# Performance work log

Measured on AMD Instinct MI355X. Metric: run time of the kernel, lower is better.

## Reference

```python
import jax, jax.numpy as jnp
import numpy as np

L = 2          # num_layers
D = 2048       # embed_dim
HQ = 16        # num_q_heads
HK = 4         # num_kv_heads
HD = D // HQ   # head_size = 128
G = HQ // HK   # q_to_kv_ratio = 4
P = 8192       # embed_dim_proj
V = 32000      # vocab_size
B = 1
S = 2048
EPS = 1e-5
THETA = 500000.0
NEG = -1e30


def setup_inputs() -> dict:
    key = jax.random.key(0)
    ks = jax.random.split(key, 8)
    s = 0.02
    return {
        "tokens": jax.random.randint(ks[0], (B, S), 0, V, dtype=jnp.int32),
        "embed": jax.random.normal(ks[1], (V, D), jnp.float32) * s,
        "attn_norm_w": jnp.ones((L, D), jnp.float32),
        "qkv_w": jax.random.normal(ks[2], (L, D, D + 2 * HK * HD), jnp.float32) * s,
        "attn_out_w": jax.random.normal(ks[3], (L, D, D), jnp.float32) * s,
        "mlp_norm_w": jnp.ones((L, D), jnp.float32),
        "mlp_in_w": jax.random.normal(ks[4], (L, D, 2 * P), jnp.float32) * s,
        "mlp_out_w": jax.random.normal(ks[5], (L, P, D), jnp.float32) * s,
        "final_norm_w": jnp.ones((D,), jnp.float32),
        "lm_head_w": jax.random.normal(ks[6], (D, V), jnp.float32) * s,
    }


def _rms(x, w):
    return w * (x * jax.lax.rsqrt(jnp.mean(x * x, axis=-1, keepdims=True) + EPS))


def _rope_cos_sin():
    inv = 1.0 / (THETA ** (jnp.arange(0, HD, 2, dtype=jnp.float32) / HD))  # [HD/2]
    ang = jnp.arange(S, dtype=jnp.float32)[:, None] * inv[None, :]         # [S, HD/2]
    return jnp.cos(ang), jnp.sin(ang)


def _rope(t, cos, sin):
    # t: [B,S,H,HD]; interleaved complex rotation on (even, odd) pairs
    x = t.reshape(t.shape[:-1] + (HD // 2, 2))
    x0, x1 = x[..., 0], x[..., 1]
    c = cos[None, :, None, :]
    sn = sin[None, :, None, :]
    out = jnp.stack([x0 * c - x1 * sn, x0 * sn + x1 * c], axis=-1)
    return out.reshape(t.shape)


def _layer(x, nw1, wqkv, wo, nw2, wi, wmo, cos, sin, mask):
    # attention block (pre-norm, residual)
    h = _rms(x, nw1)
    qkv = h @ wqkv
    q = qkv[..., :D].reshape(B, S, HQ, HD)
    k = qkv[..., D:D + HK * HD].reshape(B, S, HK, HD)
    v = qkv[..., D + HK * HD:].reshape(B, S, HK, HD)
    q = _rope(q, cos, sin)
    k = _rope(k, cos, sin)
    # GQA: repeat_interleave along head dim
    k = jnp.repeat(k, G, axis=2)
    v = jnp.repeat(v, G, axis=2)
    scores = jnp.einsum('bqhd,bkhd->bhqk', q, k) / np.float32(np.sqrt(HD))
    scores = jnp.where(mask, scores, NEG)
    attn = jax.nn.softmax(scores, axis=-1)
    o = jnp.einsum('bhqk,bkhd->bqhd', attn, v).reshape(B, S, D)
    x = x + o @ wo
    # SwiGLU block (pre-norm, residual)
    h = _rms(x, nw2)
    gu = h @ wi
    gate, up = gu[..., :P], gu[..., P:]
    x = x + (jax.nn.silu(gate) * up) @ wmo
    return x


def reference(tokens, embed, attn_norm_w, qkv_w, attn_out_w, mlp_norm_w,
              mlp_in_w, mlp_out_w, final_norm_w, lm_head_w):
    cos, sin = _rope_cos_sin()
    mask = jnp.tril(jnp.ones((S, S), dtype=bool))  # offset=0 prefill -> causal
    x = embed[tokens]  # [B,S,D]
    for i in range(L):
        x = _layer(x, attn_norm_w[i], qkv_w[i], attn_out_w[i],
                   mlp_norm_w[i], mlp_in_w[i], mlp_out_w[i], cos, sin, mask)
    return _rms(x, final_norm_w) @ lm_head_w  # [B,S,V]
```

## Files before the change

kernel.cpp:

```cpp
#include <hip/hip_runtime.h>
#include <math.h>

#define S_LEN 2048
#define DMODEL 2048
#define NHQ 16
#define NHK 4
#define HDIM 128
#define PDIM 8192
#define VOCAB 32000
#define NQKV 3072
#define EPSI 1e-5f

typedef unsigned short u16;
typedef unsigned int u32;
typedef __bf16 bf16x8 __attribute__((ext_vector_type(8)));
typedef float f32x4 __attribute__((ext_vector_type(4)));

__device__ __forceinline__ u16 f2bf(float f){
  u32 u = __builtin_bit_cast(u32, f);
  u += 0x7fffu + ((u >> 16) & 1u);
  return (u16)(u >> 16);
}
__device__ __forceinline__ float bf2f(u16 h){
  u32 u = ((u32)h) << 16;
  return __builtin_bit_cast(float, u);
}
__device__ __forceinline__ bf16x8 ld8(const u16* p){
  return __builtin_bit_cast(bf16x8, *(const uint4*)p);
}
__device__ __forceinline__ f32x4 mfma16(bf16x8 a, bf16x8 b, f32x4 c){
  return __builtin_amdgcn_mfma_f32_16x16x32_bf16(a, b, c, 0, 0, 0);
}

#define GLOAD_LDS16(gp, lp) __builtin_amdgcn_global_load_lds( \
    (__attribute__((address_space(1))) void*)(gp), \
    (__attribute__((address_space(3))) void*)(lp), 16, 0, 0)

__device__ __forceinline__ bf16x8 lds_frag(const u16* Lb, int R, int g){
  const int Rp = R >> 1;
  const int s8 = (((R & 1) << 2) | g) ^ (Rp & 7);
  return ld8(Lb + Rp * 64 + s8 * 8);
}
__device__ __forceinline__ void stage_sw(const u16* base, long row0, int kstride, int kt,
                                         int q, u16* Ldst_waveuniform){
  const int Rp = q >> 3;
  const int u = (q & 7) ^ (Rp & 7);
  const int R = (Rp << 1) | (u >> 2);
  const u16* gp = base + (row0 + R) * (long)kstride + kt + ((u & 3) << 3);
  GLOAD_LDS16(gp, Ldst_waveuniform);
}

__device__ __forceinline__ void map_bmn(int id0, int nwg, int nbn, int G,
                                        int& bm, int& bn){
  const int cpx = nwg >> 3;
  const int id = (id0 & 7) * cpx + (id0 >> 3);
  const int bmi = id % G;
  const int r2 = id / G;
  bn = r2 % nbn;
  bm = (r2 / nbn) * G + bmi;
}

__global__ void k_embed(const int* __restrict__ tok, const float* __restrict__ emb,
                        float* __restrict__ x){
  const int s = blockIdx.x, t = threadIdx.x;
  const long r = tok[s];
  const float4* src = (const float4*)(emb + r * DMODEL);
  float4* dst = (float4*)(x + (long)s * DMODEL);
  dst[t] = src[t];
  dst[t + 256] = src[t + 256];
}

__global__ void k_rmsnorm(const float* __restrict__ x, const float* __restrict__ w,
                          u16* __restrict__ out){
  const int s = blockIdx.x, t = threadIdx.x;
  const float4* xr = (const float4*)(x + (long)s * DMODEL);
  const float4 a = xr[t], b = xr[t + 256];
  float ss = a.x*a.x + a.y*a.y + a.z*a.z + a.w*a.w
           + b.x*b.x + b.y*b.y + b.z*b.z + b.w*b.w;
  #pragma unroll
  for (int off = 32; off > 0; off >>= 1) ss += __shfl_down(ss, off, 64);
  __shared__ float part[4];
  if ((t & 63) == 0) part[t >> 6] = ss;
  __syncthreads();
  const float r = rsqrtf((part[0] + part[1] + part[2] + part[3]) * (1.f / 2048.f) + EPSI);
  const float4* wr = (const float4*)w;
  const float4 wa = wr[t], wb = wr[t + 256];
  uint2 ua, ub;
  ua.x = (u32)f2bf(a.x*r*wa.x) | ((u32)f2bf(a.y*r*wa.y) << 16);
  ua.y = (u32)f2bf(a.z*r*wa.z) | ((u32)f2bf(a.w*r*wa.w) << 16);
  ub.x = (u32)f2bf(b.x*r*wb.x) | ((u32)f2bf(b.y*r*wb.y) << 16);
  ub.y = (u32)f2bf(b.z*r*wb.z) | ((u32)f2bf(b.w*r*wb.w) << 16);
  *(uint2*)(out + (long)s * DMODEL + 4 * t) = ua;
  *(uint2*)(out + (long)s * DMODEL + 1024 + 4 * t) = ub;
}

__global__ __launch_bounds__(256) void k_convT(const float* __restrict__ W,
                                               u16* __restrict__ Wt, int N, int K){
  const int n0 = blockIdx.x * 64, k0 = blockIdx.y * 64;
  const int t = threadIdx.x;
  __shared__ u16 T[64][72];
  const int r = t >> 4, c = (t & 15) << 2;
  #pragma unroll
  for (int p = 0; p < 4; ++p){
    const int k = p * 16 + r;
    const float4 v = *(const float4*)(W + (long)(k0 + k) * N + n0 + c);
    T[c + 0][k] = f2bf(v.x);
    T[c + 1][k] = f2bf(v.y);
    T[c + 2][k] = f2bf(v.z);
    T[c + 3][k] = f2bf(v.w);
  }
  __syncthreads();
  const int nr = t >> 3, kc = (t & 7) << 3;
  #pragma unroll
  for (int p = 0; p < 2; ++p){
    const int n = p * 32 + nr;
    *(uint4*)(Wt + (long)(n0 + n) * K + k0 + kc) = *(const uint4*)(&T[n][kc]);
  }
}

__global__ __launch_bounds__(256) void k_convTmi(const float* __restrict__ W,
                                                 u16* __restrict__ Wt, int N, int K){
  const int n0 = blockIdx.x * 64, k0 = blockIdx.y * 64;
  const int t = threadIdx.x;
  __shared__ u16 T[64][72];
  const int r = t >> 4, c = (t & 15) << 2;
  #pragma unroll
  for (int p = 0; p < 4; ++p){
    const int k = p * 16 + r;
    const float4 v = *(const float4*)(W + (long)(k0 + k) * N + n0 + c);
    T[c + 0][k] = f2bf(v.x);
    T[c + 1][k] = f2bf(v.y);
    T[c + 2][k] = f2bf(v.z);
    T[c + 3][k] = f2bf(v.w);
  }
  __syncthreads();
  int drow0;
  if (n0 < PDIM) drow0 = (n0 >> 7) * 256 + (n0 & 127);
  else { const int m0 = n0 - PDIM; drow0 = (m0 >> 7) * 256 + 128 + (m0 & 127); }
  const int nr = t >> 3, kc = (t & 7) << 3;
  #pragma unroll
  for (int p = 0; p < 2; ++p){
    const int n = p * 32 + nr;
    *(uint4*)(Wt + (long)(drow0 + n) * K + k0 + kc) = *(const uint4*)(&T[n][kc]);
  }
}

__global__ __launch_bounds__(256) void k_transV(const u16* __restrict__ qkv,
                                                u16* __restrict__ vT){
  const int s0 = blockIdx.x * 64, d0 = blockIdx.y * 64, kh = blockIdx.z;
  const int t = threadIdx.x;
  __shared__ u16 T[64][72];
  #pragma unroll
  for (int p = 0; p < 4; ++p){
    const int s = p * 16 + (t >> 4);
    const int c = (t & 15) * 4;
    const uint2 v = *(const uint2*)(qkv + (long)(s0 + s) * NQKV + DMODEL + 512 + kh * HDIM + d0 + c);
    T[c + 0][s] = (u16)(v.x);
    T[c + 1][s] = (u16)(v.x >> 16);
    T[c + 2][s] = (u16)(v.y);
    T[c + 3][s] = (u16)(v.y >> 16);
  }
  __syncthreads();
  #pragma unroll
  for (int p = 0; p < 2; ++p){
    const int d = p * 32 + (t >> 3);
    *(uint4*)(vT + ((long)kh * HDIM + d0 + d) * S_LEN + s0 + (t & 7) * 8) =
        *(const uint4*)(&T[d][(t & 7) * 8]);
  }
}

template<int OUT_BF16, int RES>
__global__ __launch_bounds__(256) void k_gemm(const u16* __restrict__ A, const u16* __restrict__ Bt,
                                              void* C, const float* Rs,
                                              int M, int N, int K, int nbn, int G){
  int bm, bn;
  map_bmn(blockIdx.x, gridDim.x, nbn, G, bm, bn);
  const int t = threadIdx.x;
  const int w = t >> 6, lane = t & 63, l15 = lane & 15, g = lane >> 4;
  const int wr = w >> 1, wc = w & 1;
  __shared__ u16 As[4096];
  __shared__ u16 Bs[4096];
  f32x4 acc[4][4] = {};
  const long arow = (long)bm * 128;
  const long brow = (long)bn * 128;
  for (int kt = 0; kt < K; kt += 32){
    __syncthreads();
    #pragma unroll
    for (int c = 0; c < 2; ++c){
      const int q0 = ((w << 1) | c) << 6;
      const int q  = q0 | lane;
      stage_sw(A,  arow, K, kt, q, As + q0 * 8);
      stage_sw(Bt, brow, K, kt, q, Bs + q0 * 8);
    }
    __syncthreads();
    bf16x8 af[4], bfr[4];
    #pragma unroll
    for (int i = 0; i < 4; ++i)
      af[i] = lds_frag(As, wr * 64 + i * 16 + l15, g);
    #pragma unroll
    for (int i = 0; i < 4; ++i)
      bfr[i] = lds_frag(Bs, wc * 64 + i * 16 + l15, g);
    #pragma unroll
    for (int mi = 0; mi < 4; ++mi)
      #pragma unroll
      for (int ni = 0; ni < 4; ++ni)
        acc[mi][ni] = mfma16(af[mi], bfr[ni], acc[mi][ni]);
  }
  const int row0 = bm * 128 + wr * 64, col0 = bn * 128 + wc * 64;
  #pragma unroll
  for (int mi = 0; mi < 4; ++mi){
    #pragma unroll
    for (int ni = 0; ni < 4; ++ni){
      #pragma unroll
      for (int r = 0; r < 4; ++r){
        const long ri = row0 + mi * 16 + g * 4 + r;
        const long ci = col0 + ni * 16 + l15;
        float v = acc[mi][ni][r];
        if (RES) v += Rs[ri * N + ci];
        if (OUT_BF16) ((u16*)C)[ri * N + ci] = f2bf(v);
        else          ((float*)C)[ri * N + ci] = v;
      }
    }
  }
}

__global__ __launch_bounds__(256) void k_gemmsk(const u16* __restrict__ A,
                                                const u16* __restrict__ Bt,
                                                float* __restrict__ P,
                                                int M, int N, int K, int nbn, int G){
  const int ks = blockIdx.y;
  const int KH = K >> 1;
  A  += (long)ks * KH;
  Bt += (long)ks * KH;
  P  += (long)ks * M * N;
  int bm, bn;
  map_bmn(blockIdx.x, gridDim.x, nbn, G, bm, bn);
  const int t = threadIdx.x;
  const int w = t >> 6, lane = t & 63, l15 = lane & 15, g = lane >> 4;
  const int wr = w >> 1, wc = w & 1;
  __shared__ u16 As[4096];
  __shared__ u16 Bs[4096];
  f32x4 acc[4][4] = {};
  const long arow = (long)bm * 128;
  const long brow = (long)bn * 128;
  for (int kt = 0; kt < KH; kt += 32){
    __syncthreads();
    #pragma unroll
    for (int c = 0; c < 2; ++c){
      const int q0 = ((w << 1) | c) << 6;
      const int q  = q0 | lane;
      stage_sw(A,  arow, K, kt, q, As + q0 * 8);
      stage_sw(Bt, brow, K, kt, q, Bs + q0 * 8);
    }
    __syncthreads();
    bf16x8 af[4], bfr[4];
    #pragma unroll
    for (int i = 0; i < 4; ++i)
      af[i] = lds_frag(As, wr * 64 + i * 16 + l15, g);
    #pragma unroll
    for (int i = 0; i < 4; ++i)
      bfr[i] = lds_frag(Bs, wc * 64 + i * 16 + l15, g);
    #pragma unroll
    for (int mi = 0; mi < 4; ++mi)
      #pragma unroll
      for (int ni = 0; ni < 4; ++ni)
        acc[mi][ni] = mfma16(af[mi], bfr[ni], acc[mi][ni]);
  }
  const int row0 = bm * 128 + wr * 64, col0 = bn * 128 + wc * 64;
  #pragma unroll
  for (int mi = 0; mi < 4; ++mi){
    #pragma unroll
    for (int ni = 0; ni < 4; ++ni){
      #pragma unroll
      for (int r = 0; r < 4; ++r){
        const long ri = row0 + mi * 16 + g * 4 + r;
        const long ci = col0 + ni * 16 + l15;
        P[ri * N + ci] = acc[mi][ni][r];
      }
    }
  }
}

__global__ void k_red2(float* __restrict__ x, const float* __restrict__ p0,
                       const float* __restrict__ p1){
  const long i = ((long)blockIdx.x * 256 + threadIdx.x) * 4;
  const float4 a = *(const float4*)(p0 + i);
  const float4 b = *(const float4*)(p1 + i);
  float4 c = *(const float4*)(x + i);
  c.x += a.x + b.x; c.y += a.y + b.y; c.z += a.z + b.z; c.w += a.w + b.w;
  *(float4*)(x + i) = c;
}

template<int OUT_BF16>
__global__ __launch_bounds__(1024, 4) void k_gemmX(const u16* __restrict__ A,
                                                   const u16* __restrict__ Bt,
                                                   void* C, int M, int N, int K){
  __shared__ u16 L[65536];
  const int t = threadIdx.x;
  const int w = t >> 6, lane = t & 63, l15 = lane & 15, g = lane >> 4;
  const int wr = w >> 2, wc = w & 3;
  const int nbm = M >> 8;
  int id = blockIdx.x;
  {
    const int cpx = gridDim.x >> 3;
    id = (id & 7) * cpx + (id >> 3);
  }
  const int bm = id % nbm, bn = id / nbm;
  const int NT = K >> 5;

  const int Rp0 = t >> 3;
  const int u0  = (t & 7) ^ (Rp0 & 7);
  const int R0  = (Rp0 << 1) | (u0 >> 2);
  const int kc0 = (u0 & 3) << 3;
  const u16* pA = A  + ((long)bm * 256 + R0) * (long)K + kc0;
  const u16* pB = Bt + ((long)bn * 256 + R0) * (long)K + kc0;
  const int w0 = (t & ~63) * 8;

  auto stage = [&](int s){
    u16* d = L + s * 16384;
    GLOAD_LDS16(pA, d + w0);
    GLOAD_LDS16(pB, d + 8192 + w0);
    pA += 32; pB += 32;
  };

  stage(0); stage(1); stage(2);
  asm volatile("s_waitcnt vmcnt(4)" ::: "memory");
  __builtin_amdgcn_s_barrier();

  f32x4 acc[4][4] = {};
  for (int tt = 0; tt < NT; ++tt){
    const int slot = tt & 3;
    const u16* sA = L + slot * 16384;
    const u16* sB = sA + 8192;
    bf16x8 af[4], bfr[4];
    #pragma unroll
    for (int mi = 0; mi < 4; ++mi)
      af[mi] = lds_frag(sA, wr * 64 + mi * 16 + l15, g);
    #pragma unroll
    for (int ni = 0; ni < 4; ++ni)
      bfr[ni] = lds_frag(sB, wc * 64 + ni * 16 + l15, g);
    if (tt + 3 < NT) stage((tt + 3) & 3);
    asm volatile("s_waitcnt lgkmcnt(0)" ::: "memory");
    if (tt + 3 < NT)      asm volatile("s_waitcnt vmcnt(4)" ::: "memory");
    else if (tt + 2 < NT) asm volatile("s_waitcnt vmcnt(2)" ::: "memory");
    else if (tt + 1 < NT) asm volatile("s_waitcnt vmcnt(0)" ::: "memory");
    __builtin_amdgcn_s_barrier();
    __builtin_amdgcn_s_setprio(1);
    #pragma unroll
    for (int mi = 0; mi < 4; ++mi)
      #pragma unroll
      for (int ni = 0; ni < 4; ++ni)
        acc[mi][ni] = mfma16(af[mi], bfr[ni], acc[mi][ni]);
    __builtin_amdgcn_s_setprio(0);
  }
  const int row0 = bm * 256 + wr * 64, col0 = bn * 256 + wc * 64;
  #pragma unroll
  for (int mi = 0; mi < 4; ++mi){
    #pragma unroll
    for (int ni = 0; ni < 4; ++ni){
      #pragma unroll
      for (int r = 0; r < 4; ++r){
        const long ri = row0 + mi * 16 + g * 4 + r;
        const long ci = col0 + ni * 16 + l15;
        const float v = acc[mi][ni][r];
        if (OUT_BF16) ((u16*)C)[ri * N + ci] = f2bf(v);
        else          ((float*)C)[ri * N + ci] = v;
      }
    }
  }
}

__global__ __launch_bounds__(1024, 4) void k_gemmXswi(const u16* __restrict__ A,
                                                      const u16* __restrict__ Bt,
                                                      u16* __restrict__ O,
                                                      int M, int K){
  __shared__ u16 L[65536];
  const int t = threadIdx.x;
  const int w = t >> 6, lane = t & 63, l15 = lane & 15, g = lane >> 4;
  const int wr = w >> 2, wc = w & 3;
  const int nbm = M >> 8;
  int id = blockIdx.x;
  {
    const int cpx = gridDim.x >> 3;
    id = (id & 7) * cpx + (id >> 3);
  }
  const int bm = id % nbm, bn = id / nbm;
  const int NT = K >> 5;

  const int Rp0 = t >> 3;
  const int u0  = (t & 7) ^ (Rp0 & 7);
  const int R0  = (Rp0 << 1) | (u0 >> 2);
  const int kc0 = (u0 & 3) << 3;
  const u16* pA = A  + ((long)bm * 256 + R0) * (long)K + kc0;
  const u16* pB = Bt + ((long)bn * 256 + R0) * (long)K + kc0;
  const int w0 = (t & ~63) * 8;

  auto stage = [&](int s){
    u16* d = L + s * 16384;
    GLOAD_LDS16(pA, d + w0);
    GLOAD_LDS16(pB, d + 8192 + w0);
    pA += 32; pB += 32;
  };

  stage(0); stage(1); stage(2);
  asm volatile("s_waitcnt vmcnt(4)" ::: "memory");
  __builtin_amdgcn_s_barrier();

  f32x4 acc[4][4] = {};
  for (int tt = 0; tt < NT; ++tt){
    const int slot = tt & 3;
    const u16* sA = L + slot * 16384;
    const u16* sB = sA + 8192;
    bf16x8 af[4], bfr[4];
    #pragma unroll
    for (int mi = 0; mi < 4; ++mi)
      af[mi] = lds_frag(sA, wr * 64 + mi * 16 + l15, g);
    #pragma unroll
    for (int ni = 0; ni < 4; ++ni)
      bfr[ni] = lds_frag(sB, wc * 64 + ni * 16 + l15, g);
    if (tt + 3 < NT) stage((tt + 3) & 3);
    asm volatile("s_waitcnt lgkmcnt(0)" ::: "memory");
    if (tt + 3 < NT)      asm volatile("s_waitcnt vmcnt(4)" ::: "memory");
    else if (tt + 2 < NT) asm volatile("s_waitcnt vmcnt(2)" ::: "memory");
    else if (tt + 1 < NT) asm volatile("s_waitcnt vmcnt(0)" ::: "memory");
    __builtin_amdgcn_s_barrier();
    __builtin_amdgcn_s_setprio(1);
    #pragma unroll
    for (int mi = 0; mi < 4; ++mi)
      #pragma unroll
      for (int ni = 0; ni < 4; ++ni)
        acc[mi][ni] = mfma16(af[mi], bfr[ni], acc[mi][ni]);
    __builtin_amdgcn_s_setprio(0);
  }
  __syncthreads();
  float* U = (float*)L;
  if (wc >= 2){
    const int base = ((wr << 1) | (wc - 2)) * 4096;
    #pragma unroll
    for (int mi = 0; mi < 4; ++mi)
      #pragma unroll
      for (int ni = 0; ni < 4; ++ni)
        #pragma unroll
        for (int r = 0; r < 4; ++r)
          U[base + (mi * 16 + g * 4 + r) * 64 + ni * 16 + l15] = acc[mi][ni][r];
  }
  __syncthreads();
  if (wc < 2){
    const int base = ((wr << 1) | wc) * 4096;
    #pragma unroll
    for (int mi = 0; mi < 4; ++mi){
      #pragma unroll
      for (int ni = 0; ni < 4; ++ni){
        #pragma unroll
        for (int r = 0; r < 4; ++r){
          const float gv = acc[mi][ni][r];
          const float uv = U[base + (mi * 16 + g * 4 + r) * 64 + ni * 16 + l15];
          const float ov = gv / (1.f + __expf(-gv)) * uv;
          const long ri = bm * 256 + wr * 64 + mi * 16 + g * 4 + r;
          const int ci = bn * 128 + wc * 64 + ni * 16 + l15;
          O[ri * PDIM + ci] = f2bf(ov);
        }
      }
    }
  }
}

__global__ void k_rope(u16* __restrict__ qkv){
  const int idx = blockIdx.x * 256 + threadIdx.x;
  const int i = idx & 63;
  const int head = (idx >> 6) % 20;
  const int s = idx / (64 * 20);
  const long base = (long)s * NQKV + (head < NHQ ? head * HDIM : DMODEL + (head - NHQ) * HDIM);
  u32* p = (u32*)(qkv + base + 2 * i);
  const u32 v = *p;
  const float x0 = bf2f((u16)(v & 0xffffu)), x1 = bf2f((u16)(v >> 16));
  const float ang = (float)s * exp2f(-0.29580575889569023f * (float)i);
  float sn, cs;
  sincosf(ang, &sn, &cs);
  const float y0 = x0 * cs - x1 * sn;
  const float y1 = x0 * sn + x1 * cs;
  *p = (u32)f2bf(y0) | ((u32)f2bf(y1) << 16);
}

__global__ __launch_bounds__(512) void k_attn(const u16* __restrict__ qkv,
                                              const u16* __restrict__ vT,
                                              u16* __restrict__ o){
  const int qb = blockIdx.x;
  const int kh = blockIdx.y >> 1;
  const int h  = (kh << 2) + ((blockIdx.y & 1) << 1) + (threadIdx.x >> 8);
  const int t = threadIdx.x, lane = t & 63, l15 = lane & 15, g = lane >> 4;
  const int ws = (t >> 6) & 3;
  const int wv = t >> 6;
  __shared__ u16 Ks[2][8192];
  __shared__ u16 Vs[2][8192];
  __shared__ u16 Ps[8][16 * 72];
  const int q0 = qb * 64 + ws * 16;
  bf16x8 aq[4];
  #pragma unroll
  for (int d0 = 0; d0 < 4; ++d0)
    aq[d0] = ld8(qkv + (long)(q0 + l15) * NQKV + h * HDIM + d0 * 32 + g * 8);
  f32x4 acc_o[8] = {};
  float mst[4], lst[4];
  #pragma unroll
  for (int r = 0; r < 4; ++r){ mst[r] = -1e30f; lst[r] = 0.f; }
  const float scale = 0.08838834764831843f;

  auto stageK = [&](int kt, int b){
    #pragma unroll
    for (int p = 0; p < 2; ++p){
      const int q = p * 512 + t;
      const int r = q >> 4, u = q & 15;
      const u16* gp = qkv + (long)(kt * 64 + r) * NQKV + DMODEL + kh * HDIM + ((u ^ (r & 15)) << 3);
      GLOAD_LDS16(gp, Ks[b] + (p * 512 + (t & ~63)) * 8);
    }
  };
  auto stageV = [&](int kt, int b){
    #pragma unroll
    for (int p = 0; p < 2; ++p){
      const int q = p * 512 + t;
      const int r = q >> 3, u = q & 7;
      const u16* gp = vT + ((long)kh * HDIM + r) * S_LEN + kt * 64 + ((u ^ (r & 7)) << 3);
      GLOAD_LDS16(gp, Vs[b] + (p * 512 + (t & ~63)) * 8);
    }
  };

  const int nkt = qb + 1;
  stageK(0, 0); stageV(0, 0);
  for (int kt = 0; kt < nkt; ++kt){
    const int kv0 = kt << 6;
    __builtin_amdgcn_s_barrier();
    if (kt + 1 < nkt){
      stageK(kt + 1, (kt + 1) & 1);
      stageV(kt + 1, (kt + 1) & 1);
      asm volatile("s_waitcnt vmcnt(4)" ::: "memory");
    } else {
      asm volatile("s_waitcnt vmcnt(0)" ::: "memory");
    }
    __builtin_amdgcn_s_barrier();
    const u16* K_ = Ks[kt & 1];
    const u16* V_ = Vs[kt & 1];
    f32x4 sacc[4] = {};
    #pragma unroll
    for (int d0 = 0; d0 < 4; ++d0){
      #pragma unroll
      for (int j2 = 0; j2 < 4; ++j2){
        const bf16x8 bk = ld8(K_ + (j2 * 16 + l15) * 128 + ((((d0 << 2) | g) ^ l15) << 3));
        sacc[j2] = mfma16(aq[d0], bk, sacc[j2]);
      }
    }
    float p[4][4], scl[4];
    #pragma unroll
    for (int r = 0; r < 4; ++r){
      const int qrow = q0 + g * 4 + r;
      float mx = -1e30f;
      #pragma unroll
      for (int j2 = 0; j2 < 4; ++j2){
        float sv = sacc[j2][r] * scale;
        sv = (kv0 + j2 * 16 + l15 <= qrow) ? sv : -1e30f;
        p[j2][r] = sv;
        mx = fmaxf(mx, sv);
      }
      #pragma unroll
      for (int off = 1; off < 16; off <<= 1) mx = fmaxf(mx, __shfl_xor(mx, off, 64));
      const float mnew = fmaxf(mst[r], mx);
      scl[r] = __expf(mst[r] - mnew);
      float rs = 0.f;
      #pragma unroll
      for (int j2 = 0; j2 < 4; ++j2){ p[j2][r] = __expf(p[j2][r] - mnew); rs += p[j2][r]; }
      #pragma unroll
      for (int off = 1; off < 16; off <<= 1) rs += __shfl_xor(rs, off, 64);
      lst[r] = lst[r] * scl[r] + rs;
      mst[r] = mnew;
    }
    #pragma unroll
    for (int n = 0; n < 8; ++n)
      #pragma unroll
      for (int r = 0; r < 4; ++r)
        acc_o[n][r] *= scl[r];
    #pragma unroll
    for (int j2 = 0; j2 < 4; ++j2)
      #pragma unroll
      for (int r = 0; r < 4; ++r)
        Ps[wv][(g * 4 + r) * 72 + j2 * 16 + l15] = f2bf(p[j2][r]);
    #pragma unroll
    for (int kk = 0; kk < 2; ++kk){
      const bf16x8 pa = ld8(Ps[wv] + l15 * 72 + kk * 32 + g * 8);
      #pragma unroll
      for (int n = 0; n < 8; ++n){
        const int row = n * 16 + l15;
        const bf16x8 bv = ld8(V_ + row * 64 + ((((kk << 2) | g) ^ (l15 & 7)) << 3));
        acc_o[n] = mfma16(pa, bv, acc_o[n]);
      }
    }
    asm volatile("s_waitcnt lgkmcnt(0)" ::: "memory");
  }
  #pragma unroll
  for (int n = 0; n < 8; ++n){
    #pragma unroll
    for (int r = 0; r < 4; ++r){
      const float ov = acc_o[n][r] / lst[r];
      o[(long)(q0 + g * 4 + r) * DMODEL + h * HDIM + n * 16 + l15] = f2bf(ov);
    }
  }
}

extern "C" void kernel_launch(void* const* d_in, const int* in_sizes, int n_in,
                              void* d_out, int out_size, void* d_ws, size_t ws_size,
                              hipStream_t stream){
  const int*   tokens       = (const int*)d_in[0];
  const float* embed        = (const float*)d_in[1];
  const float* attn_norm_w  = (const float*)d_in[2];
  const float* qkv_w        = (const float*)d_in[3];
  const float* attn_out_w   = (const float*)d_in[4];
  const float* mlp_norm_w   = (const float*)d_in[5];
  const float* mlp_in_w     = (const float*)d_in[6];
  const float* mlp_out_w    = (const float*)d_in[7];
  const float* final_norm_w = (const float*)d_in[8];
  const float* lm_head_w    = (const float*)d_in[9];

  char* ws = (char*)d_ws;
  float* xf  = (float*)(ws);
  u16* hbf   = (u16*)(ws + 16777216);
  u16* qkvb  = (u16*)(ws + 25165824);
  u16* obf   = (u16*)(ws + 37748736);
  u16* gub   = (u16*)(ws + 46137344);
  u16* hb2   = (u16*)(ws + 113246208);
  u16* wbuf  = (u16*)(ws + 146800640);
  u16* vTb   = (u16*)(ws + 277872640);
  float* pp  = (float*)gub;

  k_embed<<<S_LEN, 256, 0, stream>>>(tokens, embed, xf);
  for (int l = 0; l < 2; ++l){
    k_rmsnorm<<<S_LEN, 256, 0, stream>>>(xf, attn_norm_w + (long)l * DMODEL, hbf);
    k_convT<<<dim3(NQKV/64, DMODEL/64), 256, 0, stream>>>(
        qkv_w + (long)l * DMODEL * NQKV, wbuf, NQKV, DMODEL);
    k_gemm<1,0><<<(S_LEN/128) * (NQKV/128), 256, 0, stream>>>(
        hbf, wbuf, qkvb, nullptr, S_LEN, NQKV, DMODEL, NQKV/128, 4);
    k_rope<<<(S_LEN * 20 * 64) / 256, 256, 0, stream>>>(qkvb);
    k_transV<<<dim3(S_LEN/64, 2, 4), 256, 0, stream>>>(qkvb, vTb);
    k_attn<<<dim3(S_LEN/64, 8), 512, 0, stream>>>(qkvb, vTb, obf);
    k_convT<<<dim3(DMODEL/64, DMODEL/64), 256, 0, stream>>>(
        attn_out_w + (long)l * DMODEL * DMODEL, wbuf, DMODEL, DMODEL);
    k_gemm<0,1><<<(S_LEN/128) * (DMODEL/128), 256, 0, stream>>>(
        obf, wbuf, xf, xf, S_LEN, DMODEL, DMODEL, DMODEL/128, 4);
    k_rmsnorm<<<S_LEN, 256, 0, stream>>>(xf, mlp_norm_w + (long)l * DMODEL, hbf);
    k_convTmi<<<dim3((2*PDIM)/64, DMODEL/64), 256, 0, stream>>>(
        mlp_in_w + (long)l * DMODEL * 2 * PDIM, wbuf, 2*PDIM, DMODEL);
    k_gemmXswi<<<(S_LEN/256) * ((2*PDIM)/256), 1024, 0, stream>>>(
        hbf, wbuf, hb2, S_LEN, DMODEL);
    k_convT<<<dim3(DMODEL/64, PDIM/64), 256, 0, stream>>>(
        mlp_out_w + (long)l * PDIM * DMODEL, wbuf, DMODEL, PDIM);
    k_gemmsk<<<dim3((S_LEN/128) * (DMODEL/128), 2), 256, 0, stream>>>(
        hb2, wbuf, pp, S_LEN, DMODEL, PDIM, DMODEL/128, 2);
    k_red2<<<(S_LEN * DMODEL) / 1024, 256, 0, stream>>>(
        xf, pp, pp + (long)S_LEN * DMODEL);
  }
  k_rmsnorm<<<S_LEN, 256, 0, stream>>>(xf, final_norm_w, hbf);
  k_convT<<<dim3(VOCAB/64, DMODEL/64), 256, 0, stream>>>(lm_head_w, wbuf, VOCAB, DMODEL);
  k_gemmX<0><<<(S_LEN/256) * (VOCAB/256), 1024, 0, stream>>>(
      hbf, wbuf, (float*)d_out, S_LEN, VOCAB, DMODEL);
}
```

Measured before the change: 1.388 ms.

## Fuse split-K reduction with RMSNorm and reshape attention grid

Merges the split-K partial-sum reduction after the MLP-out GEMM with the following RMSNorm, whether that is the next layer's attention norm or the final norm. This removes a kernel launch and a re-read of the residual stream. Separately, attention blocks shrink to 256 threads, each handling one head. The grid becomes 1D: block IDs are interleaved so each XCD stays on one KV head, and query blocks are issued longest-first to balance causal work. Each block now stages K/V tiles alone, so K/V traffic per head pair doubles, but occupancy and scheduling granularity should improve.

```diff
diff --git a/kernel.cpp b/kernel.cpp
--- a/kernel.cpp
+++ b/kernel.cpp
@@ -92,6 +92,40 @@
   ub.y = (u32)f2bf(b.z*r*wb.z) | ((u32)f2bf(b.w*r*wb.w) << 16);
   *(uint2*)(out + (long)s * DMODEL + 4 * t) = ua;
   *(uint2*)(out + (long)s * DMODEL + 1024 + 4 * t) = ub;
+}
+
+__global__ void k_red2rms(float* __restrict__ x, const float* __restrict__ p0,
+                          const float* __restrict__ p1, const float* __restrict__ w,
+                          u16* __restrict__ out){
+  const int s = blockIdx.x, t = threadIdx.x;
+  const long base = (long)s * DMODEL;
+  float4 a = ((const float4*)(x + base))[t];
+  float4 b = ((const float4*)(x + base))[t + 256];
+  const float4 a0 = ((const float4*)(p0 + base))[t];
+  const float4 b0 = ((const float4*)(p0 + base))[t + 256];
+  const float4 a1 = ((const float4*)(p1 + base))[t];
+  const float4 b1 = ((const float4*)(p1 + base))[t + 256];
+  a.x += a0.x + a1.x; a.y += a0.y + a1.y; a.z += a0.z + a1.z; a.w += a0.w + a1.w;
+  b.x += b0.x + b1.x; b.y += b0.y + b1.y; b.z += b0.z + b1.z; b.w += b0.w + b1.w;
+  ((float4*)(x + base))[t] = a;
+  ((float4*)(x + base))[t + 256] = b;
+  float ss = a.x*a.x + a.y*a.y + a.z*a.z + a.w*a.w
+           + b.x*b.x + b.y*b.y + b.z*b.z + b.w*b.w;
+  #pragma unroll
+  for (int off = 32; off > 0; off >>= 1) ss += __shfl_down(ss, off, 64);
+  __shared__ float part[4];
+  if ((t & 63) == 0) part[t >> 6] = ss;
+  __syncthreads();
+  const float r = rsqrtf((part[0] + part[1] + part[2] + part[3]) * (1.f / 2048.f) + EPSI);
+  const float4* wr = (const float4*)w;
+  const float4 wa = wr[t], wb = wr[t + 256];
+  uint2 ua, ub;
+  ua.x = (u32)f2bf(a.x*r*wa.x) | ((u32)f2bf(a.y*r*wa.y) << 16);
+  ua.y = (u32)f2bf(a.z*r*wa.z) | ((u32)f2bf(a.w*r*wa.w) << 16);
+  ub.x = (u32)f2bf(b.x*r*wb.x) | ((u32)f2bf(b.y*r*wb.y) << 16);
+  ub.y = (u32)f2bf(b.z*r*wb.z) | ((u32)f2bf(b.w*r*wb.w) << 16);
+  *(uint2*)(out + base + 4 * t) = ua;
+  *(uint2*)(out + base + 1024 + 4 * t) = ub;
 }
 
 __global__ __launch_bounds__(256) void k_convT(const float* __restrict__ W,
@@ -281,16 +315,6 @@
   }
 }
 
-__global__ void k_red2(float* __restrict__ x, const float* __restrict__ p0,
-                       const float* __restrict__ p1){
-  const long i = ((long)blockIdx.x * 256 + threadIdx.x) * 4;
-  const float4 a = *(const float4*)(p0 + i);
-  const float4 b = *(const float4*)(p1 + i);
-  float4 c = *(const float4*)(x + i);
-  c.x += a.x + b.x; c.y += a.y + b.y; c.z += a.z + b.z; c.w += a.w + b.w;
-  *(float4*)(x + i) = c;
-}
-
 template<int OUT_BF16>
 __global__ __launch_bounds__(1024, 4) void k_gemmX(const u16* __restrict__ A,
                                                    const u16* __restrict__ Bt,
@@ -482,19 +506,19 @@
   *p = (u32)f2bf(y0) | ((u32)f2bf(y1) << 16);
 }
 
-__global__ __launch_bounds__(512) void k_attn(const u16* __restrict__ qkv,
+__global__ __launch_bounds__(256) void k_attn(const u16* __restrict__ qkv,
                                               const u16* __restrict__ vT,
                                               u16* __restrict__ o){
-  const int qb = blockIdx.x;
-  const int kh = blockIdx.y >> 1;
-  const int h  = (kh << 2) + ((blockIdx.y & 1) << 1) + (threadIdx.x >> 8);
-  const int t = threadIdx.x, lane = t & 63, l15 = lane & 15, g = lane >> 4;
-  const int ws = (t >> 6) & 3;
-  const int wv = t >> 6;
+  const int id = blockIdx.x;
+  const int xcd = id & 7, j = id >> 3;
+  const int kh = xcd >> 1;
+  const int h  = (kh << 2) + ((xcd & 1) << 1) + (j & 1);
+  const int qb = 31 - (j >> 1);
+  const int t = threadIdx.x, w = t >> 6, lane = t & 63, l15 = lane & 15, g = lane >> 4;
   __shared__ u16 Ks[2][8192];
   __shared__ u16 Vs[2][8192];
-  __shared__ u16 Ps[8][16 * 72];
-  const int q0 = qb * 64 + ws * 16;
+  __shared__ u16 Ps[4][16 * 72];
+  const int q0 = qb * 64 + w * 16;
   bf16x8 aq[4];
   #pragma unroll
   for (int d0 = 0; d0 < 4; ++d0)
@@ -507,20 +531,20 @@
 
   auto stageK = [&](int kt, int b){
     #pragma unroll
-    for (int p = 0; p < 2; ++p){
-      const int q = p * 512 + t;
+    for (int p = 0; p < 4; ++p){
+      const int q = p * 256 + t;
       const int r = q >> 4, u = q & 15;
       const u16* gp = qkv + (long)(kt * 64 + r) * NQKV + DMODEL + kh * HDIM + ((u ^ (r & 15)) << 3);
-      GLOAD_LDS16(gp, Ks[b] + (p * 512 + (t & ~63)) * 8);
+      GLOAD_LDS16(gp, Ks[b] + (p * 256 + (t & ~63)) * 8);
     }
   };
   auto stageV = [&](int kt, int b){
     #pragma unroll
-    for (int p = 0; p < 2; ++p){
-      const int q = p * 512 + t;
+    for (int p = 0; p < 4; ++p){
+      const int q = p * 256 + t;
       const int r = q >> 3, u = q & 7;
       const u16* gp = vT + ((long)kh * HDIM + r) * S_LEN + kt * 64 + ((u ^ (r & 7)) << 3);
-      GLOAD_LDS16(gp, Vs[b] + (p * 512 + (t & ~63)) * 8);
+      GLOAD_LDS16(gp, Vs[b] + (p * 256 + (t & ~63)) * 8);
     }
   };
 
@@ -532,7 +556,7 @@
     if (kt + 1 < nkt){
       stageK(kt + 1, (kt + 1) & 1);
       stageV(kt + 1, (kt + 1) & 1);
-      asm volatile("s_waitcnt vmcnt(4)" ::: "memory");
+      asm volatile("s_waitcnt vmcnt(8)" ::: "memory");
     } else {
       asm volatile("s_waitcnt vmcnt(0)" ::: "memory");
     }
@@ -581,10 +605,10 @@
     for (int j2 = 0; j2 < 4; ++j2)
       #pragma unroll
       for (int r = 0; r < 4; ++r)
-        Ps[wv][(g * 4 + r) * 72 + j2 * 16 + l15] = f2bf(p[j2][r]);
+        Ps[w][(g * 4 + r) * 72 + j2 * 16 + l15] = f2bf(p[j2][r]);
     #pragma unroll
     for (int kk = 0; kk < 2; ++kk){
-      const bf16x8 pa = ld8(Ps[wv] + l15 * 72 + kk * 32 + g * 8);
+      const bf16x8 pa = ld8(Ps[w] + l15 * 72 + kk * 32 + g * 8);
       #pragma unroll
       for (int n = 0; n < 8; ++n){
         const int row = n * 16 + l15;
@@ -630,15 +654,15 @@
   float* pp  = (float*)gub;
 
   k_embed<<<S_LEN, 256, 0, stream>>>(tokens, embed, xf);
+  k_rmsnorm<<<S_LEN, 256, 0, stream>>>(xf, attn_norm_w, hbf);
   for (int l = 0; l < 2; ++l){
-    k_rmsnorm<<<S_LEN, 256, 0, stream>>>(xf, attn_norm_w + (long)l * DMODEL, hbf);
     k_convT<<<dim3(NQKV/64, DMODEL/64), 256, 0, stream>>>(
         qkv_w + (long)l * DMODEL * NQKV, wbuf, NQKV, DMODEL);
     k_gemm<1,0><<<(S_LEN/128) * (NQKV/128), 256, 0, stream>>>(
         hbf, wbuf, qkvb, nullptr, S_LEN, NQKV, DMODEL, NQKV/128, 4);
     k_rope<<<(S_LEN * 20 * 64) / 256, 256, 0, stream>>>(qkvb);
     k_transV<<<dim3(S_LEN/64, 2, 4), 256, 0, stream>>>(qkvb, vTb);
-    k_attn<<<dim3(S_LEN/64, 8), 512, 0, stream>>>(qkvb, vTb, obf);
+    k_attn<<<512, 256, 0, stream>>>(qkvb, vTb, obf);
     k_convT<<<dim3(DMODEL/64, DMODEL/64), 256, 0, stream>>>(
         attn_out_w + (long)l * DMODEL * DMODEL, wbuf, DMODEL, DMODEL);
     k_gemm<0,1><<<(S_LEN/128) * (DMODEL/128), 256, 0, stream>>>(
@@ -652,10 +676,10 @@
         mlp_out_w + (long)l * PDIM * DMODEL, wbuf, DMODEL, PDIM);
     k_gemmsk<<<dim3((S_LEN/128) * (DMODEL/128), 2), 256, 0, stream>>>(
         hb2, wbuf, pp, S_LEN, DMODEL, PDIM, DMODEL/128, 2);
-    k_red2<<<(S_LEN * DMODEL) / 1024, 256, 0, stream>>>(
-        xf, pp, pp + (long)S_LEN * DMODEL);
-  }
-  k_rmsnorm<<<S_LEN, 256, 0, stream>>>(xf, final_norm_w, hbf);
+    k_red2rms<<<S_LEN, 256, 0, stream>>>(
+        xf, pp, pp + (long)S_LEN * DMODEL,
+        (l == 0) ? (attn_norm_w + DMODEL) : final_norm_w, hbf);
+  }
   k_convT<<<dim3(VOCAB/64, DMODEL/64), 256, 0, stream>>>(lm_head_w, wbuf, VOCAB, DMODEL);
   k_gemmX<0><<<(S_LEN/256) * (VOCAB/256), 1024, 0, stream>>>(
       hbf, wbuf, (float*)d_out, S_LEN, VOCAB, DMODEL);
```

After: 1.374 ms. No clear change (-1.0%).
